# Kernel tuning notes

Hardware: AMD Instinct MI355X
Metric: run time of the kernel (lower is better)

The kernel has to match this reference:

```python
import jax, jax.numpy as jnp
import numpy as np

N = 100000
E = 1600000
IN_FEATS = 512
DIMS = [128, 128, 64]
NEG_SLOPE_ATT = 0.2   # PyG GATConv default
NEG_SLOPE_ACT = 0.25  # F.leaky_relu in GAT.forward


def setup_inputs() -> dict:
    key = jax.random.key(0)
    ks = jax.random.split(key, 16)
    inp = {
        "data": jax.random.normal(ks[0], (N, IN_FEATS), dtype=jnp.float32),
        "adj": jax.random.randint(ks[1], (2, E), 0, N, dtype=jnp.int64),
    }
    dims_in = [IN_FEATS] + DIMS[:-1]
    ki = 2
    for l, (di, do) in enumerate(zip(dims_in, DIMS), start=1):
        scale = 1.0 / np.sqrt(di)
        inp[f"W{l}"] = jax.random.normal(ks[ki], (di, do), dtype=jnp.float32) * scale; ki += 1
        inp[f"a_src{l}"] = jax.random.normal(ks[ki], (do,), dtype=jnp.float32) * 0.1; ki += 1
        inp[f"a_dst{l}"] = jax.random.normal(ks[ki], (do,), dtype=jnp.float32) * 0.1; ki += 1
        inp[f"b{l}"] = jnp.zeros((do,), dtype=jnp.float32)
    return inp


def gat_conv(x, src, dst, W, a_src, a_dst, b):
    h = x @ W                                        # [N, do]
    alpha_s = h @ a_src                              # [N]
    alpha_d = h @ a_dst                              # [N]
    logits = jax.nn.leaky_relu(alpha_s[src] + alpha_d[dst], NEG_SLOPE_ATT)  # [E']
    # segment softmax over edges sharing the same destination node
    m = jax.ops.segment_max(logits, dst, num_segments=N)
    e = jnp.exp(logits - m[dst])
    s = jax.ops.segment_sum(e, dst, num_segments=N)
    alpha = e / s[dst]                               # [E']
    out = jax.ops.segment_sum(alpha[:, None] * h[src], dst, num_segments=N)
    return out + b


def reference(data, adj, W1, a_src1, a_dst1, b1, W2, a_src2, a_dst2, b2, W3, a_src3, a_dst3, b3):
    # PyG GATConv adds self-loops by default
    loops = jnp.arange(N, dtype=adj.dtype)
    src = jnp.concatenate([adj[0], loops])
    dst = jnp.concatenate([adj[1], loops])
    x = data
    x = jax.nn.leaky_relu(gat_conv(x, src, dst, W1, a_src1, a_dst1, b1), NEG_SLOPE_ACT)
    x = jax.nn.leaky_relu(gat_conv(x, src, dst, W2, a_src2, a_dst2, b2), NEG_SLOPE_ACT)
    x = jax.nn.leaky_relu(gat_conv(x, src, dst, W3, a_src3, a_dst3, b3), NEG_SLOPE_ACT)
    return x
```

## Files before the change

### kernel.cpp

```cpp
#include <hip/hip_runtime.h>

typedef unsigned short u16;
typedef unsigned int u32;
typedef short short8 __attribute__((ext_vector_type(8)));
typedef float floatx4 __attribute__((ext_vector_type(4)));

__device__ __forceinline__ float bf2f(u16 x) { return __uint_as_float(((u32)x) << 16); }
__device__ __forceinline__ u16 f2bf(float x) {
    u32 u = __float_as_uint(x);
    u += 0x7fffu + ((u >> 16) & 1u);
    return (u16)(u >> 16);
}

__global__ void zero_out_k(float* __restrict__ out, int n) {
    int i = blockIdx.x * 256 + threadIdx.x;
    if (i < n) out[i] = 0.f;
}


__global__ void hist_k(const int* __restrict__ dst, int* __restrict__ cnt, int E, int N) {
    int e = blockIdx.x * 256 + threadIdx.x;
    if (e < E) {
        int d = dst[e];
        d = d < 0 ? 0 : (d >= N ? N - 1 : d);
        atomicAdd(&cnt[d], 1);
    }
}

__global__ void scan1_k(const int* __restrict__ cnt, int* __restrict__ excl,
                        int* __restrict__ aux, int N) {
    __shared__ int tmp[1024];
    int t = threadIdx.x;
    int i = blockIdx.x * 1024 + t;
    int v = (i < N) ? cnt[i] : 0;
    tmp[t] = v;
    __syncthreads();
    for (int off = 1; off < 1024; off <<= 1) {
        int x = (t >= off) ? tmp[t - off] : 0;
        __syncthreads();
        tmp[t] += x;
        __syncthreads();
    }
    if (i < N) excl[i] = tmp[t] - v;
    if (t == 1023) aux[blockIdx.x] = tmp[t];
}

__global__ void scan2_k(int* __restrict__ aux, int nb) {
    int lane = threadIdx.x;
    int v0 = (lane < nb) ? aux[lane] : 0;
    int v1 = (lane + 64 < nb) ? aux[lane + 64] : 0;
    int s0 = v0;
    for (int off = 1; off < 64; off <<= 1) { int x = __shfl_up(s0, off); if (lane >= off) s0 += x; }
    int total0 = __shfl(s0, 63);
    int s1 = v1;
    for (int off = 1; off < 64; off <<= 1) { int x = __shfl_up(s1, off); if (lane >= off) s1 += x; }
    if (lane < nb) aux[lane] = s0 - v0;
    if (lane + 64 < nb) aux[lane + 64] = total0 + s1 - v1;
}

__global__ void scan3_k(const int* __restrict__ excl, const int* __restrict__ aux,
                        int* __restrict__ offs, int* __restrict__ cursor, int N, int E) {
    int i = blockIdx.x * 1024 + threadIdx.x;
    if (i < N) {
        int v = excl[i] + aux[blockIdx.x];
        offs[i] = v;
        cursor[i] = v;
    } else if (i == N) {
        offs[N] = E;
    }
}

__global__ void scatter_k(const int* __restrict__ src, const int* __restrict__ dst,
                          int* __restrict__ cursor, int* __restrict__ esrc, int E, int N) {
    int e = blockIdx.x * 256 + threadIdx.x;
    if (e < E) {
        int d = dst[e];
        d = d < 0 ? 0 : (d >= N ? N - 1 : d);
        int s = src[e];
        s = s < 0 ? 0 : (s >= N ? N - 1 : s);
        int p = atomicAdd(&cursor[d], 1);
        esrc[p] = s;
    }
}

__global__ void prepack_k(const float* __restrict__ W, u16* __restrict__ Wf, int DO, int total) {
    int idx = blockIdx.x * 256 + threadIdx.x;
    if (idx >= total) return;
    int j = idx & 7;
    int t = idx >> 3;
    int n = t % DO;
    int kq = t / DO;
    Wf[idx] = f2bf(W[(size_t)(kq * 8 + j) * DO + n]);
}

template <int K, int DO, bool F32IN, bool H32>
__global__ __launch_bounds__(256, 2) void gemm_k(const void* __restrict__ Xv,
                                                 const u16* __restrict__ Wf,
                                                 void* __restrict__ Hv,
                                                 const float* __restrict__ a_src,
                                                 const float* __restrict__ a_dst,
                                                 float* __restrict__ AS,
                                                 float* __restrict__ AD, int nrow) {
    constexpr int BM = 128, BK = 64;
    __shared__ alignas(16) u16 At[BM * BK];
    const int tid = threadIdx.x;
    const int wave = tid >> 6, lane = tid & 63;
    const int quad = lane >> 4, l16 = lane & 15;
    const int row0 = blockIdx.x * BM;

    floatx4 acc[2][DO / 16];
#pragma unroll
    for (int a = 0; a < 2; a++)
#pragma unroll
        for (int b = 0; b < DO / 16; b++) acc[a][b] = floatx4{0.f, 0.f, 0.f, 0.f};

    for (int kt = 0; kt < K / BK; ++kt) {
        __syncthreads();
#pragma unroll
        for (int i = 0; i < 4; ++i) {
            int seg = tid + i * 256;
            int r = seg >> 3, c = seg & 7;
            int gr = row0 + r;
            gr = gr < nrow ? gr : nrow - 1;
            u16 pk[8];
            if (F32IN) {
                const float* X = (const float*)Xv;
                float4 v0 = *(const float4*)(X + (size_t)gr * K + kt * BK + c * 8);
                float4 v1 = *(const float4*)(X + (size_t)gr * K + kt * BK + c * 8 + 4);
                pk[0] = f2bf(v0.x); pk[1] = f2bf(v0.y); pk[2] = f2bf(v0.z); pk[3] = f2bf(v0.w);
                pk[4] = f2bf(v1.x); pk[5] = f2bf(v1.y); pk[6] = f2bf(v1.z); pk[7] = f2bf(v1.w);
                *(int4*)(At + r * BK + (c ^ (r & 7)) * 8) = *(const int4*)pk;
            } else {
                const u16* X = (const u16*)Xv;
                int4 v = *(const int4*)(X + (size_t)gr * K + kt * BK + c * 8);
                *(int4*)(At + r * BK + (c ^ (r & 7)) * 8) = v;
            }
        }
        __syncthreads();
#pragma unroll
        for (int ks = 0; ks < 2; ++ks) {
            short8 bfr[DO / 16];
            int kq = kt * 8 + ks * 4 + quad;
#pragma unroll
            for (int ct = 0; ct < DO / 16; ++ct)
                bfr[ct] = *(const short8*)(Wf + ((size_t)kq * DO + ct * 16 + l16) * 8);
#pragma unroll
            for (int rt = 0; rt < 2; ++rt) {
                int row = wave * 32 + rt * 16 + l16;
                int unit = (ks * 4 + quad) ^ (row & 7);
                short8 afr = *(const short8*)(At + row * BK + unit * 8);
#pragma unroll
                for (int ct = 0; ct < DO / 16; ++ct)
                    acc[rt][ct] =
                        __builtin_amdgcn_mfma_f32_16x16x32_bf16(afr, bfr[ct], acc[rt][ct], 0, 0, 0);
            }
        }
    }
    float asv[DO / 16], adv[DO / 16];
#pragma unroll
    for (int ct = 0; ct < DO / 16; ++ct) {
        asv[ct] = a_src[ct * 16 + l16];
        adv[ct] = a_dst[ct * 16 + l16];
    }
#pragma unroll
    for (int rt = 0; rt < 2; ++rt)
#pragma unroll
        for (int r = 0; r < 4; ++r) {
            int grow = row0 + wave * 32 + rt * 16 + quad * 4 + r;
            bool ok = grow < nrow;
            float ps = 0.f, pd = 0.f;
#pragma unroll
            for (int ct = 0; ct < DO / 16; ++ct) {
                float v = acc[rt][ct][r];
                ps = fmaf(v, asv[ct], ps);
                pd = fmaf(v, adv[ct], pd);
                if (ok) {
                    if (H32)
                        ((float*)Hv)[(size_t)grow * DO + ct * 16 + l16] = v;
                    else
                        ((u16*)Hv)[(size_t)grow * DO + ct * 16 + l16] = f2bf(v);
                }
            }
#pragma unroll
            for (int o = 1; o < 16; o <<= 1) {
                ps += __shfl_xor(ps, o);
                pd += __shfl_xor(pd, o);
            }
            if (ok && l16 == 0) {
                AS[grow] = ps;
                AD[grow] = pd;
            }
        }
}

template <int DO, bool HB, bool OUTB>
__global__ __launch_bounds__(256) void agg_k(const void* __restrict__ Hv,
                                             const float* __restrict__ AS,
                                             const float* __restrict__ AD,
                                             const int* __restrict__ offs,
                                             const int* __restrict__ esrc,
                                             const float* __restrict__ bias,
                                             void* __restrict__ OUT, int N) {
    const int wave = threadIdx.x >> 6, lane = threadIdx.x & 63;
    const int d = blockIdx.x * 4 + wave;
    if (d >= N) return;
    const int o0 = offs[d];
    const int deg = offs[d + 1] - o0;
    const int tot = deg + 1;
    const float ad = AD[d];

    float acc0 = 0.f, acc1 = 0.f;

    if (tot <= 64) {
        int s = (lane < deg) ? esrc[o0 + lane] : d;
        bool valid = lane < tot;
        float lg = AS[s] + ad;
        lg = lg > 0.f ? lg : lg * 0.2f;
        float lgv = valid ? lg : -1e30f;
        float m = lgv;
        for (int o = 32; o; o >>= 1) m = fmaxf(m, __shfl_xor(m, o));
        float e = valid ? __expf(lg - m) : 0.f;
        float sum = e;
        for (int o = 32; o; o >>= 1) sum += __shfl_xor(sum, o);
        float w = e * (1.f / sum);
        for (int l = 0; l < tot; ++l) {
            float wl = __shfl(w, l);
            int sl = __shfl(s, l);
            if (DO == 128) {
                if (HB) {
                    u32 hv = ((const u32*)Hv)[(size_t)sl * 64 + lane];
                    acc0 = fmaf(wl, bf2f((u16)hv), acc0);
                    acc1 = fmaf(wl, bf2f((u16)(hv >> 16)), acc1);
                } else {
                    float2 hv = ((const float2*)Hv)[(size_t)sl * 64 + lane];
                    acc0 = fmaf(wl, hv.x, acc0);
                    acc1 = fmaf(wl, hv.y, acc1);
                }
            } else {
                if (HB) {
                    acc0 = fmaf(wl, bf2f(((const u16*)Hv)[(size_t)sl * DO + lane]), acc0);
                } else {
                    acc0 = fmaf(wl, ((const float*)Hv)[(size_t)sl * DO + lane], acc0);
                }
            }
        }
    } else {
        float mx = -1e30f;
        for (int i = lane; i < tot; i += 64) {
            int s = (i < deg) ? esrc[o0 + i] : d;
            float lg = AS[s] + ad;
            lg = lg > 0.f ? lg : lg * 0.2f;
            mx = fmaxf(mx, lg);
        }
        for (int o = 32; o; o >>= 1) mx = fmaxf(mx, __shfl_xor(mx, o));
        float sum = 0.f;
        for (int i = lane; i < tot; i += 64) {
            int s = (i < deg) ? esrc[o0 + i] : d;
            float lg = AS[s] + ad;
            lg = lg > 0.f ? lg : lg * 0.2f;
            sum += __expf(lg - mx);
        }
        for (int o = 32; o; o >>= 1) sum += __shfl_xor(sum, o);
        const float inv = 1.f / sum;
        for (int c0 = 0; c0 < tot; c0 += 64) {
            int i = c0 + lane;
            float w = 0.f;
            int s = d;
            if (i < tot) {
                s = (i < deg) ? esrc[o0 + i] : d;
                float lg = AS[s] + ad;
                lg = lg > 0.f ? lg : lg * 0.2f;
                w = __expf(lg - mx) * inv;
            }
            int cn = tot - c0;
            cn = cn < 64 ? cn : 64;
            for (int l = 0; l < cn; ++l) {
                float wl = __shfl(w, l);
                int sl = __shfl(s, l);
                if (DO == 128) {
                    if (HB) {
                        u32 hv = ((const u32*)Hv)[(size_t)sl * 64 + lane];
                        acc0 = fmaf(wl, bf2f((u16)hv), acc0);
                        acc1 = fmaf(wl, bf2f((u16)(hv >> 16)), acc1);
                    } else {
                        float2 hv = ((const float2*)Hv)[(size_t)sl * 64 + lane];
                        acc0 = fmaf(wl, hv.x, acc0);
                        acc1 = fmaf(wl, hv.y, acc1);
                    }
                } else {
                    if (HB) {
                        acc0 = fmaf(wl, bf2f(((const u16*)Hv)[(size_t)sl * DO + lane]), acc0);
                    } else {
                        acc0 = fmaf(wl, ((const float*)Hv)[(size_t)sl * DO + lane], acc0);
                    }
                }
            }
        }
    }

    if (DO == 128) {
        int f = 2 * lane;
        float v0 = acc0 + bias[f];
        float v1 = acc1 + bias[f + 1];
        v0 = v0 > 0.f ? v0 : v0 * 0.25f;
        v1 = v1 > 0.f ? v1 : v1 * 0.25f;
        if (OUTB) {
            u32 packed = (u32)f2bf(v0) | ((u32)f2bf(v1) << 16);
            ((u32*)OUT)[(size_t)d * 64 + lane] = packed;
        } else {
            ((float2*)OUT)[(size_t)d * 64 + lane] = float2{v0, v1};
        }
    } else {
        float v0 = acc0 + bias[lane];
        v0 = v0 > 0.f ? v0 : v0 * 0.25f;
        if (OUTB) {
            ((u16*)OUT)[(size_t)d * DO + lane] = f2bf(v0);
        } else {
            ((float*)OUT)[(size_t)d * DO + lane] = v0;
        }
    }
}


extern "C" void kernel_launch(void* const* d_in, const int* in_sizes, int n_in,
                              void* d_out, int out_size, void* d_ws, size_t ws_size,
                              hipStream_t stream) {
    const int N = in_sizes[0] / 512;
    const int E = in_sizes[1] / 2;

    const float* data = (const float*)d_in[0];
    const int* adj = (const int*)d_in[1];
    const float* W1 = (const float*)d_in[2];
    const float* as1 = (const float*)d_in[3];
    const float* ad1 = (const float*)d_in[4];
    const float* b1 = (const float*)d_in[5];
    const float* W2 = (const float*)d_in[6];
    const float* as2 = (const float*)d_in[7];
    const float* ad2 = (const float*)d_in[8];
    const float* b2 = (const float*)d_in[9];
    const float* W3 = (const float*)d_in[10];
    const float* as3 = (const float*)d_in[11];
    const float* ad3 = (const float*)d_in[12];
    const float* b3 = (const float*)d_in[13];

    char* ws = (char*)d_ws;
    size_t need = 0;
    auto carve = [&](size_t bytes) {
        void* p = (void*)(ws + need);
        need += (bytes + 255) & ~(size_t)255;
        return p;
    };
    int* esrc = (int*)carve((size_t)E * 4);
    int* offs = (int*)carve((size_t)(N + 1) * 4);
    int* cursor = (int*)carve((size_t)N * 4);
    int* cnt = (int*)carve((size_t)N * 4);
    int* excl = (int*)carve((size_t)N * 4);
    int* aux = (int*)carve(1024);
    float* AS = (float*)carve((size_t)N * 4);
    float* AD = (float*)carve((size_t)N * 4);
    u16* Hb = (u16*)carve((size_t)N * 128 * 2);
    float* H32 = (float*)Hb;
    u16* x1 = (u16*)carve((size_t)N * 128 * 2);
    u16* x2 = x1;
    u16* Wf1 = (u16*)carve(512 * 128 * 2);
    u16* Wf2 = (u16*)carve(128 * 128 * 2);
    u16* Wf3 = (u16*)carve(128 * 64 * 2);

    if (need > ws_size) {
        zero_out_k<<<(out_size + 255) / 256, 256, 0, stream>>>((float*)d_out, out_size);
        return;
    }

    const int* srcl = adj;
    const int* dstl = adj + E;

    hipMemsetAsync(cnt, 0, (size_t)N * 4, stream);
    hist_k<<<(E + 255) / 256, 256, 0, stream>>>(dstl, cnt, E, N);
    int nb = (N + 1023) / 1024;
    scan1_k<<<nb, 1024, 0, stream>>>(cnt, excl, aux, N);
    scan2_k<<<1, 64, 0, stream>>>(aux, nb);
    scan3_k<<<nb, 1024, 0, stream>>>(excl, aux, offs, cursor, N, E);
    scatter_k<<<(E + 255) / 256, 256, 0, stream>>>(srcl, dstl, cursor, esrc, E, N);

    prepack_k<<<(512 * 128 + 255) / 256, 256, 0, stream>>>(W1, Wf1, 128, 512 * 128);
    prepack_k<<<(128 * 128 + 255) / 256, 256, 0, stream>>>(W2, Wf2, 128, 128 * 128);
    prepack_k<<<(128 * 64 + 255) / 256, 256, 0, stream>>>(W3, Wf3, 64, 128 * 64);

    const int gblk = (N + 127) / 128;
    const int nblk = (N + 3) / 4;

    gemm_k<512, 128, true, false><<<gblk, 256, 0, stream>>>(data, Wf1, Hb, as1, ad1, AS, AD, N);
    agg_k<128, true, true><<<nblk, 256, 0, stream>>>(Hb, AS, AD, offs, esrc, b1, x1, N);
    gemm_k<128, 128, false, false><<<gblk, 256, 0, stream>>>(x1, Wf2, Hb, as2, ad2, AS, AD, N);
    agg_k<128, true, true><<<nblk, 256, 0, stream>>>(Hb, AS, AD, offs, esrc, b2, x2, N);
    gemm_k<128, 64, false, true><<<gblk, 256, 0, stream>>>(x2, Wf3, H32, as3, ad3, AS, AD, N);
    agg_k<64, false, false><<<nblk, 256, 0, stream>>>(H32, AS, AD, offs, esrc, b3, d_out, N);
}
```

Baseline: 925.7 us.

## Build CSR via two-level bucketed counting sort instead of per-node global atomics

Replaces the per-node histogram, three-kernel scan and per-edge atomic scatter with a bucketed scheme. Edges are first counted into 128-node buckets using shared-memory histograms, then scattered into bucket order as (src,dst) pairs. A per-bucket kernel then builds node offsets and the final esrc with shared-memory atomics. The aim is to cut contended global atomics and random global writes during CSR construction, at the cost of an extra E*8-byte temp buffer, one more pass over the edges, and a limit of 1024 buckets.

New measurement: 1.138 ms. 1.23x slower.

```diff
diff --git a/kernel.cpp b/kernel.cpp
--- a/kernel.cpp
+++ b/kernel.cpp
@@ -17,22 +17,31 @@
     if (i < n) out[i] = 0.f;
 }
 
-
-__global__ void hist_k(const int* __restrict__ dst, int* __restrict__ cnt, int E, int N) {
-    int e = blockIdx.x * 256 + threadIdx.x;
-    if (e < E) {
+constexpr int BW = 128;
+
+__global__ void bhist_k(const int* __restrict__ dst, int* __restrict__ bcnt, int E, int N,
+                        int NB) {
+    __shared__ int h[1024];
+    for (int i = threadIdx.x; i < NB; i += 256) h[i] = 0;
+    __syncthreads();
+    int stride = gridDim.x * 256;
+    for (int e = blockIdx.x * 256 + threadIdx.x; e < E; e += stride) {
         int d = dst[e];
         d = d < 0 ? 0 : (d >= N ? N - 1 : d);
-        atomicAdd(&cnt[d], 1);
-    }
-}
-
-__global__ void scan1_k(const int* __restrict__ cnt, int* __restrict__ excl,
-                        int* __restrict__ aux, int N) {
+        atomicAdd(&h[d / BW], 1);
+    }
+    __syncthreads();
+    for (int i = threadIdx.x; i < NB; i += 256) {
+        int v = h[i];
+        if (v) atomicAdd(&bcnt[i], v);
+    }
+}
+
+__global__ void bscan_k(const int* __restrict__ bcnt, int* __restrict__ bbase,
+                        int* __restrict__ bcur, int NB, int E) {
     __shared__ int tmp[1024];
     int t = threadIdx.x;
-    int i = blockIdx.x * 1024 + t;
-    int v = (i < N) ? cnt[i] : 0;
+    int v = (t < NB) ? bcnt[t] : 0;
     tmp[t] = v;
     __syncthreads();
     for (int off = 1; off < 1024; off <<= 1) {
@@ -41,45 +50,61 @@
         tmp[t] += x;
         __syncthreads();
     }
-    if (i < N) excl[i] = tmp[t] - v;
-    if (t == 1023) aux[blockIdx.x] = tmp[t];
-}
-
-__global__ void scan2_k(int* __restrict__ aux, int nb) {
-    int lane = threadIdx.x;
-    int v0 = (lane < nb) ? aux[lane] : 0;
-    int v1 = (lane + 64 < nb) ? aux[lane + 64] : 0;
-    int s0 = v0;
-    for (int off = 1; off < 64; off <<= 1) { int x = __shfl_up(s0, off); if (lane >= off) s0 += x; }
-    int total0 = __shfl(s0, 63);
-    int s1 = v1;
-    for (int off = 1; off < 64; off <<= 1) { int x = __shfl_up(s1, off); if (lane >= off) s1 += x; }
-    if (lane < nb) aux[lane] = s0 - v0;
-    if (lane + 64 < nb) aux[lane + 64] = total0 + s1 - v1;
-}
-
-__global__ void scan3_k(const int* __restrict__ excl, const int* __restrict__ aux,
-                        int* __restrict__ offs, int* __restrict__ cursor, int N, int E) {
-    int i = blockIdx.x * 1024 + threadIdx.x;
-    if (i < N) {
-        int v = excl[i] + aux[blockIdx.x];
-        offs[i] = v;
-        cursor[i] = v;
-    } else if (i == N) {
-        offs[N] = E;
-    }
-}
-
-__global__ void scatter_k(const int* __restrict__ src, const int* __restrict__ dst,
-                          int* __restrict__ cursor, int* __restrict__ esrc, int E, int N) {
+    if (t < NB) {
+        int base = tmp[t] - v;
+        bbase[t] = base;
+        bcur[t] = base;
+    }
+    if (t == 0) bbase[NB] = E;
+}
+
+__global__ void bscatter_k(const int* __restrict__ src, const int* __restrict__ dst,
+                           int* __restrict__ bcur, uint2* __restrict__ tmp, int E, int N) {
     int e = blockIdx.x * 256 + threadIdx.x;
     if (e < E) {
         int d = dst[e];
         d = d < 0 ? 0 : (d >= N ? N - 1 : d);
         int s = src[e];
         s = s < 0 ? 0 : (s >= N ? N - 1 : s);
-        int p = atomicAdd(&cursor[d], 1);
-        esrc[p] = s;
+        int p = atomicAdd(&bcur[d / BW], 1);
+        tmp[p] = uint2{(u32)s, (u32)d};
+    }
+}
+
+__global__ __launch_bounds__(256) void csr_k(const uint2* __restrict__ tmp,
+                                             const int* __restrict__ bbase,
+                                             int* __restrict__ offs, int* __restrict__ esrc,
+                                             int N, int E, int NB) {
+    __shared__ int cnt[BW], pos[BW], sb[BW];
+    const int b = blockIdx.x;
+    const int t = threadIdx.x;
+    const int lo = bbase[b], hi = bbase[b + 1];
+    const int n0 = b * BW;
+    if (t < BW) cnt[t] = 0;
+    __syncthreads();
+    for (int i = lo + t; i < hi; i += 256) atomicAdd(&cnt[(int)tmp[i].y - n0], 1);
+    __syncthreads();
+    if (t < BW) sb[t] = cnt[t];
+    __syncthreads();
+    for (int off = 1; off < BW; off <<= 1) {
+        int v = 0;
+        if (t < BW && t >= off) v = sb[t - off];
+        __syncthreads();
+        if (t < BW) sb[t] += v;
+        __syncthreads();
+    }
+    if (t < BW) {
+        int excl = sb[t] - cnt[t];
+        pos[t] = excl;
+        int node = n0 + t;
+        if (node < N) offs[node] = lo + excl;
+    }
+    if (b == NB - 1 && t == 0) offs[N] = E;
+    __syncthreads();
+    for (int i = lo + t; i < hi; i += 256) {
+        uint2 ed = tmp[i];
+        int p = atomicAdd(&pos[(int)ed.y - n0], 1);
+        esrc[lo + p] = (int)ed.x;
     }
 }
 
@@ -327,6 +352,7 @@
                               hipStream_t stream) {
     const int N = in_sizes[0] / 512;
     const int E = in_sizes[1] / 2;
+    const int NB = (N + BW - 1) / BW;
 
     const float* data = (const float*)d_in[0];
     const int* adj = (const int*)d_in[1];
@@ -351,11 +377,11 @@
         return p;
     };
     int* esrc = (int*)carve((size_t)E * 4);
+    uint2* tmp = (uint2*)carve((size_t)E * 8);
     int* offs = (int*)carve((size_t)(N + 1) * 4);
-    int* cursor = (int*)carve((size_t)N * 4);
-    int* cnt = (int*)carve((size_t)N * 4);
-    int* excl = (int*)carve((size_t)N * 4);
-    int* aux = (int*)carve(1024);
+    int* bcnt = (int*)carve(1025 * 4);
+    int* bbase = (int*)carve(1025 * 4);
+    int* bcur = (int*)carve(1025 * 4);
     float* AS = (float*)carve((size_t)N * 4);
     float* AD = (float*)carve((size_t)N * 4);
     u16* Hb = (u16*)carve((size_t)N * 128 * 2);
@@ -366,7 +392,7 @@
     u16* Wf2 = (u16*)carve(128 * 128 * 2);
     u16* Wf3 = (u16*)carve(128 * 64 * 2);
 
-    if (need > ws_size) {
+    if (need > ws_size || NB > 1024) {
         zero_out_k<<<(out_size + 255) / 256, 256, 0, stream>>>((float*)d_out, out_size);
         return;
     }
@@ -374,13 +400,11 @@
     const int* srcl = adj;
     const int* dstl = adj + E;
 
-    hipMemsetAsync(cnt, 0, (size_t)N * 4, stream);
-    hist_k<<<(E + 255) / 256, 256, 0, stream>>>(dstl, cnt, E, N);
-    int nb = (N + 1023) / 1024;
-    scan1_k<<<nb, 1024, 0, stream>>>(cnt, excl, aux, N);
-    scan2_k<<<1, 64, 0, stream>>>(aux, nb);
-    scan3_k<<<nb, 1024, 0, stream>>>(excl, aux, offs, cursor, N, E);
-    scatter_k<<<(E + 255) / 256, 256, 0, stream>>>(srcl, dstl, cursor, esrc, E, N);
+    hipMemsetAsync(bcnt, 0, 1025 * 4, stream);
+    bhist_k<<<512, 256, 0, stream>>>(dstl, bcnt, E, N, NB);
+    bscan_k<<<1, 1024, 0, stream>>>(bcnt, bbase, bcur, NB, E);
+    bscatter_k<<<(E + 255) / 256, 256, 0, stream>>>(srcl, dstl, bcur, tmp, E, N);
+    csr_k<<<NB, 256, 0, stream>>>(tmp, bbase, offs, esrc, N, E, NB);
 
     prepack_k<<<(512 * 128 + 255) / 256, 256, 0, stream>>>(W1, Wf1, 128, 512 * 128);
     prepack_k<<<(128 * 128 + 255) / 256, 256, 0, stream>>>(W2, Wf2, 128, 128 * 128);
```
